# Kernel optimization log

Measured on AMD Instinct MI355X. Metric: run time of the kernel, lower is better.

## Reference

```python
import jax, jax.numpy as jnp
import numpy as np

INPUT_SIZE = 512
HIDDEN_SIZE = 1024
SEQ_LEN = 512
BATCH = 64

def _xavier(key, shape):
    fan_out, fan_in = shape
    bound = float(np.sqrt(6.0 / (fan_in + fan_out)))
    return jax.random.uniform(key, shape, jnp.float32, -bound, bound)

def setup_inputs() -> dict:
    key = jax.random.key(0)
    ks = jax.random.split(key, 5)
    return {
        "x_seq": jax.random.normal(ks[0], (SEQ_LEN, BATCH, INPUT_SIZE), jnp.float32),
        "h0": jax.random.normal(ks[1], (BATCH, HIDDEN_SIZE), jnp.float32),
        "U_c": _xavier(ks[2], (HIDDEN_SIZE, INPUT_SIZE)),
        "w_c": jnp.ones((HIDDEN_SIZE,), jnp.float32),
        "b_c": jnp.zeros((HIDDEN_SIZE,), jnp.float32),
        "U_a": _xavier(ks[3], (HIDDEN_SIZE, INPUT_SIZE)),
        "w_a": jnp.ones((HIDDEN_SIZE,), jnp.float32),
        "b_a": jnp.zeros((HIDDEN_SIZE,), jnp.float32),
        "U_h": _xavier(ks[4], (HIDDEN_SIZE, INPUT_SIZE)),
        "b_h": jnp.zeros((HIDDEN_SIZE,), jnp.float32),
    }

def reference(x_seq, h0, U_c, w_c, b_c, U_a, w_a, b_a, U_h, b_h):
    # Batch the three input projections across all timesteps (the compute-heavy
    # GEMMs), then run the inherently-sequential gated recurrence with lax.scan.
    xc = jnp.einsum('tbi,hi->tbh', x_seq, U_c) + b_c  # [T, B, H]
    xa = jnp.einsum('tbi,hi->tbh', x_seq, U_a) + b_a
    xh = jnp.einsum('tbi,hi->tbh', x_seq, U_h) + b_h

    def step(h, proj):
        pc, pa, ph = proj
        c = jax.nn.sigmoid(pc + w_c * h)
        a = 1.0 + jnp.tanh(pa + w_a * h)
        h_new = c * h + (1.0 - c) * jnp.tanh(ph + a * h)
        return h_new, h_new

    h_last, y_seq = jax.lax.scan(step, h0, (xc, xa, xh))
    return (y_seq, (h_last,))
```

## Files before the change

### kernel.cpp

```cpp
#include <hip/hip_runtime.h>
#include <cstdint>
#include <cstddef>

#define T_SEQ 512
#define BATCH 64
#define IN_SZ 512
#define HID   1024
#define BH    (BATCH*HID)
#define M_TOT (T_SEQ*BATCH)
#define D_CH  16

typedef float f32x4 __attribute__((ext_vector_type(4)));
typedef _Float16 f16x8 __attribute__((ext_vector_type(8)));

__device__ inline unsigned short f2h(float f){
  union { _Float16 h; unsigned short u; } v;
  v.h = (_Float16)f;
  return v.u;
}
__device__ inline float h2f(unsigned short s){
  union { unsigned short u; _Float16 h; } v; v.u = s;
  return (float)v.h;
}

__device__ inline float sigm_f(float x){ return 1.f/(1.f + __expf(-x)); }
__device__ inline float tanh_f(float x){ float e = __expf(2.f*x); return 1.f - 2.f/(e + 1.f); }

__device__ inline void async16(const void* g, void* l){
  __builtin_amdgcn_global_load_lds(
      (__attribute__((address_space(1))) void*)g,
      (__attribute__((address_space(3))) void*)l,
      16, 0, 0);
}

#define XBLK 16384
__global__ __launch_bounds__(256) void cvt_all(
    const float* __restrict__ x,  const float* __restrict__ Uc,
    const float* __restrict__ Ua, const float* __restrict__ Uh,
    unsigned short* __restrict__ xb, unsigned short* __restrict__ U0,
    unsigned short* __restrict__ U1, unsigned short* __restrict__ U2)
{
  int b = blockIdx.x;
  const float* in; unsigned short* out; int i;
  if (b < XBLK){
    in = x; out = xb; i = b*256 + threadIdx.x;
  } else {
    int r = b - XBLK;
    int which = r >> 9;
    int lb = r & 511;
    i = lb*256 + threadIdx.x;
    in  = (which==0) ? Uc : (which==1) ? Ua : Uh;
    out = (which==0) ? U0 : (which==1) ? U1 : U2;
  }
  float4 v = ((const float4*)in)[i];
  ushort4 o;
  o.x = f2h(v.x); o.y = f2h(v.y); o.z = f2h(v.z); o.w = f2h(v.w);
  ((ushort4*)out)[i] = o;
}

__global__ __launch_bounds__(256) void gemm3(
    const unsigned short* __restrict__ xb,
    const unsigned short* __restrict__ U0,
    const unsigned short* __restrict__ U1,
    const unsigned short* __restrict__ U2,
    const float* __restrict__ b0, const float* __restrict__ b1, const float* __restrict__ b2,
    unsigned short* out0, unsigned short* out1, void* out2, int ph_f16)
{
  __shared__ __align__(16) unsigned char smem_raw[34816];
  uint4* smem = (uint4*)smem_raw;
  unsigned short* strans = (unsigned short*)smem_raw;

  const int tid  = threadIdx.x;
  const int wave = tid >> 6, lane = tid & 63;
  const int quad = lane >> 4, l16 = lane & 15;

  const int bid  = blockIdx.x;
  const int xcd  = bid & 7;
  const int slot = bid >> 3;
  const int mbl  = slot / 24;
  const int inner = slot - mbl*24;
  const int mb = xcd*32 + mbl;
  const int z  = inner % 3;
  const int nb = inner / 3;

  const int m0 = mb * 128, n0 = nb * 128;
  const unsigned short* Um = (z==0) ? U0 : (z==1) ? U1 : U2;
  const float* bias        = (z==0) ? b0 : (z==1) ? b1 : b2;
  const int wm = wave >> 1, wn = wave & 1;

  const f32x4 zf = {0.f, 0.f, 0.f, 0.f};
  f32x4 acc[4][4];
#pragma unroll
  for (int i=0;i<4;i++)
#pragma unroll
    for (int j=0;j<4;j++) acc[i][j] = zf;

  const uint4* ldsA = smem;
  const uint4* ldsB = smem + 1024;

  for (int k0 = 0; k0 < IN_SZ; k0 += 64) {
#pragma unroll
    for (int j = 0; j < 4; j++) {
      int c   = (wave*4 + j)*64 + lane;
      int row = c >> 3;
      int og  = (c & 7) ^ (row & 7);
      const unsigned short* ga = xb + (size_t)(m0 + row)*IN_SZ + k0 + og*8;
      const unsigned short* gb = Um + (size_t)(n0 + row)*IN_SZ + k0 + og*8;
      async16(ga, (void*)(smem + (size_t)(wave*4 + j)*64));
      async16(gb, (void*)(smem + 1024 + (size_t)(wave*4 + j)*64));
    }
    __syncthreads();

#pragma unroll
    for (int ks8 = 0; ks8 < 8; ks8 += 4) {
      f16x8 af[4], bfr[4];
#pragma unroll
      for (int im = 0; im < 4; im++){
        int row = wm*64 + im*16 + l16;
        int ch  = row*8 + ((ks8 + quad) ^ (row & 7));
        af[im] = *(const f16x8*)(ldsA + ch);
      }
#pragma unroll
      for (int in = 0; in < 4; in++){
        int row = wn*64 + in*16 + l16;
        int ch  = row*8 + ((ks8 + quad) ^ (row & 7));
        bfr[in] = *(const f16x8*)(ldsB + ch);
      }
#pragma unroll
      for (int im = 0; im < 4; im++)
#pragma unroll
        for (int in = 0; in < 4; in++)
          acc[im][in] = __builtin_amdgcn_mfma_f32_16x16x32_f16(af[im], bfr[in], acc[im][in], 0, 0, 0);
    }
    __syncthreads();
  }

  float bv[4];
#pragma unroll
  for (int in = 0; in < 4; in++) bv[in] = bias[n0 + wn*64 + in*16 + l16];

  if (z == 2 && !ph_f16) {
    float* o32 = (float*)out2;
#pragma unroll
    for (int im = 0; im < 4; im++)
#pragma unroll
      for (int r = 0; r < 4; r++){
        int row = m0 + wm*64 + im*16 + quad*4 + r;
        size_t rb = (size_t)row * HID;
#pragma unroll
        for (int in = 0; in < 4; in++)
          o32[rb + n0 + wn*64 + in*16 + l16] = acc[im][in][r] + bv[in];
      }
    return;
  }

  unsigned short* op = (z==0) ? out0 : (z==1) ? out1 : (unsigned short*)out2;
  const int RS = 136;
#pragma unroll
  for (int im = 0; im < 4; im++)
#pragma unroll
    for (int r = 0; r < 4; r++){
      int row = wm*64 + im*16 + quad*4 + r;
#pragma unroll
      for (int in = 0; in < 4; in++){
        int col = wn*64 + in*16 + l16;
        strans[row*RS + col] = f2h(acc[im][in][r] + bv[in]);
      }
    }
  __syncthreads();
#pragma unroll
  for (int p = 0; p < 8; p++){
    int row = (tid >> 4) + p*16;
    int c8  = tid & 15;
    uint4 v = *(const uint4*)(strans + row*RS + c8*8);
    *(uint4*)(op + (size_t)(m0 + row)*HID + n0 + c8*8) = v;
  }
}

template <bool PH16>
__global__ __launch_bounds__(256) void scan_k(
    const unsigned short* __restrict__ pc, const unsigned short* __restrict__ pa,
    const void* __restrict__ phv,
    float* __restrict__ y,
    const float* __restrict__ h0, const float* __restrict__ wc, const float* __restrict__ wa,
    float* __restrict__ hlast)
{
  const int idx  = blockIdx.x * 256 + threadIdx.x;
  const int hidx = idx & (HID - 1);
  float h = h0[idx];
  const float wcv = wc[hidx], wav = wa[hidx];
  const unsigned short* ph16 = (const unsigned short*)phv;
  const float*          ph32 = (const float*)phv;

  unsigned short cpc[D_CH], cpa[D_CH];
  unsigned short npc[D_CH], npa[D_CH];
  float cph[D_CH], nph[D_CH];
  unsigned short cph16[D_CH], nph16[D_CH];

#pragma unroll
  for (int i = 0; i < D_CH; i++){
    size_t b = (size_t)i*BH + idx;
    cpc[i] = pc[b]; cpa[i] = pa[b];
    if (PH16) cph16[i] = ph16[b]; else cph[i] = ph32[b];
  }

  constexpr int NC = T_SEQ / D_CH;
  for (int c = 0; c < NC; c++){
    const int t0 = c * D_CH;
    if (c + 1 < NC){
#pragma unroll
      for (int i = 0; i < D_CH; i++){
        size_t b = (size_t)(t0 + D_CH + i)*BH + idx;
        npc[i] = pc[b]; npa[i] = pa[b];
        if (PH16) nph16[i] = ph16[b]; else nph[i] = ph32[b];
      }
    }
#pragma unroll
    for (int i = 0; i < D_CH; i++){
      float pcv = h2f(cpc[i]);
      float pav = h2f(cpa[i]);
      float phv_ = PH16 ? h2f(cph16[i]) : cph[i];
      float cc = sigm_f(pcv + wcv*h);
      float a  = 1.f + tanh_f(pav + wav*h);
      float hc = tanh_f(phv_ + a*h);
      h = cc*h + (1.f - cc)*hc;
      y[(size_t)(t0 + i)*BH + idx] = h;
    }
    if (c + 1 < NC){
#pragma unroll
      for (int i = 0; i < D_CH; i++){
        cpc[i] = npc[i]; cpa[i] = npa[i];
        if (PH16) cph16[i] = nph16[i]; else cph[i] = nph[i];
      }
    }
  }
  hlast[idx] = h;
}

extern "C" void kernel_launch(void* const* d_in, const int* in_sizes, int n_in,
                              void* d_out, int out_size, void* d_ws, size_t ws_size,
                              hipStream_t stream)
{
  const float* x  = (const float*)d_in[0];
  const float* h0 = (const float*)d_in[1];
  const float* Uc = (const float*)d_in[2];
  const float* wc = (const float*)d_in[3];
  const float* bc = (const float*)d_in[4];
  const float* Ua = (const float*)d_in[5];
  const float* wa = (const float*)d_in[6];
  const float* ba = (const float*)d_in[7];
  const float* Uh = (const float*)d_in[8];
  const float* bh = (const float*)d_in[9];

  float* y     = (float*)d_out;
  float* hlast = y + (size_t)T_SEQ * BH;

  const size_t szP16 = (size_t)T_SEQ * BH * 2;
  const size_t szX16 = (size_t)M_TOT * IN_SZ * 2;
  const size_t szU16 = (size_t)HID * IN_SZ * 2;

  const size_t base = 2*szP16 + szX16 + 3*szU16;
  const bool ph_sep = ws_size >= base + szP16;

  char* w = (char*)d_ws;
  unsigned short* pc16 = (unsigned short*)w;
  unsigned short* pa16 = (unsigned short*)(w + szP16);
  unsigned short* xb   = (unsigned short*)(w + 2*szP16);
  unsigned short* U0b  = (unsigned short*)(w + 2*szP16 + szX16);
  unsigned short* U1b  = U0b + szU16/2;
  unsigned short* U2b  = U1b + szU16/2;
  unsigned short* ph16 = (unsigned short*)(w + base);

  cvt_all<<<XBLK + 3*512, 256, 0, stream>>>(x, Uc, Ua, Uh, xb, U0b, U1b, U2b);

  void* phbuf = ph_sep ? (void*)ph16 : (void*)y;
  gemm3<<<6144, 256, 0, stream>>>(xb, U0b, U1b, U2b, bc, ba, bh,
                                  pc16, pa16, phbuf, ph_sep ? 1 : 0);

  if (ph_sep)
    scan_k<true><<<BH/256, 256, 0, stream>>>(pc16, pa16, (const void*)ph16,
                                             y, h0, wc, wa, hlast);
  else
    scan_k<false><<<BH/256, 256, 0, stream>>>(pc16, pa16, (const void*)y,
                                              y, h0, wc, wa, hlast);
}
```

Baseline: 436.3 us.

## Rewrite projection GEMM with 256x256 tiles and double-buffered async LDS pipeline

The three-way projection GEMM moves from 128x128 tiles with 4 waves and a load-then-compute loop to 256x256 tiles with 8 waves. The K loop is now split into half-tiles and double-buffered in 128KB of LDS, with explicit vmcnt waits, barriers and raised priority around MFMA clusters. This overlaps global loads with matrix math and raises data reuse per tile. The epilogue also changes to per-wave LDS staging without a block-wide sync. It relies on hand-tuned waitcnt counts, which are fragile, and the large LDS footprint limits occupancy.

```diff
diff --git a/kernel.cpp b/kernel.cpp
--- a/kernel.cpp
+++ b/kernel.cpp
@@ -58,7 +58,7 @@
   ((ushort4*)out)[i] = o;
 }
 
-__global__ __launch_bounds__(256) void gemm3(
+__global__ __launch_bounds__(512, 2) void gemm3(
     const unsigned short* __restrict__ xb,
     const unsigned short* __restrict__ U0,
     const unsigned short* __restrict__ U1,
@@ -66,9 +66,7 @@
     const float* __restrict__ b0, const float* __restrict__ b1, const float* __restrict__ b2,
     unsigned short* out0, unsigned short* out1, void* out2, int ph_f16)
 {
-  __shared__ __align__(16) unsigned char smem_raw[34816];
-  uint4* smem = (uint4*)smem_raw;
-  unsigned short* strans = (unsigned short*)smem_raw;
+  __shared__ __align__(16) unsigned char smem_raw[131072];
 
   const int tid  = threadIdx.x;
   const int wave = tid >> 6, lane = tid & 63;
@@ -77,103 +75,153 @@
   const int bid  = blockIdx.x;
   const int xcd  = bid & 7;
   const int slot = bid >> 3;
-  const int mbl  = slot / 24;
-  const int inner = slot - mbl*24;
-  const int mb = xcd*32 + mbl;
-  const int z  = inner % 3;
-  const int nb = inner / 3;
-
-  const int m0 = mb * 128, n0 = nb * 128;
+  const int mbl  = slot / 12;
+  const int inner= slot - mbl*12;
+  const int mb   = xcd*16 + mbl;
+  const int z    = inner % 3;
+  const int nb   = inner / 3;
+
+  const int m0 = mb * 256, n0 = nb * 256;
   const unsigned short* Um = (z==0) ? U0 : (z==1) ? U1 : U2;
   const float* bias        = (z==0) ? b0 : (z==1) ? b1 : b2;
-  const int wm = wave >> 1, wn = wave & 1;
+  const int wm = wave >> 2, wn = wave & 3;
+
+  const int laneRow = lane >> 2;
+  const int cg8     = ((lane & 3) ^ ((lane >> 3) & 3)) << 3;
+  const unsigned short* srcA = xb + (size_t)m0 * IN_SZ;
+  const unsigned short* srcB = Um + (size_t)n0 * IN_SZ;
+
+  const int cxa = l16*64 + ((quad ^ ((l16 >> 1) & 3)) << 4);
+
+  auto stageA = [&](int tile, int kh){
+    unsigned char* dst = smem_raw + (((tile & 1)*2 + kh) << 14);
+#pragma unroll
+    for (int j = 0; j < 2; ++j){
+      const unsigned short* g = srcA + (size_t)((wave*2 + j)*16 + laneRow)*IN_SZ
+                                + tile*64 + kh*32 + cg8;
+      async16(g, dst + (wave*2 + j)*1024);
+    }
+  };
+  auto stageB = [&](int tile, int kh){
+    unsigned char* dst = smem_raw + 65536 + (((tile & 1)*2 + kh) << 14);
+#pragma unroll
+    for (int j = 0; j < 2; ++j){
+      const unsigned short* g = srcB + (size_t)((wave*2 + j)*16 + laneRow)*IN_SZ
+                                + tile*64 + kh*32 + cg8;
+      async16(g, dst + (wave*2 + j)*1024);
+    }
+  };
 
   const f32x4 zf = {0.f, 0.f, 0.f, 0.f};
-  f32x4 acc[4][4];
-#pragma unroll
-  for (int i=0;i<4;i++)
-#pragma unroll
-    for (int j=0;j<4;j++) acc[i][j] = zf;
-
-  const uint4* ldsA = smem;
-  const uint4* ldsB = smem + 1024;
-
-  for (int k0 = 0; k0 < IN_SZ; k0 += 64) {
-#pragma unroll
-    for (int j = 0; j < 4; j++) {
-      int c   = (wave*4 + j)*64 + lane;
-      int row = c >> 3;
-      int og  = (c & 7) ^ (row & 7);
-      const unsigned short* ga = xb + (size_t)(m0 + row)*IN_SZ + k0 + og*8;
-      const unsigned short* gb = Um + (size_t)(n0 + row)*IN_SZ + k0 + og*8;
-      async16(ga, (void*)(smem + (size_t)(wave*4 + j)*64));
-      async16(gb, (void*)(smem + 1024 + (size_t)(wave*4 + j)*64));
-    }
-    __syncthreads();
-
-#pragma unroll
-    for (int ks8 = 0; ks8 < 8; ks8 += 4) {
-      f16x8 af[4], bfr[4];
-#pragma unroll
-      for (int im = 0; im < 4; im++){
-        int row = wm*64 + im*16 + l16;
-        int ch  = row*8 + ((ks8 + quad) ^ (row & 7));
-        af[im] = *(const f16x8*)(ldsA + ch);
-      }
-#pragma unroll
-      for (int in = 0; in < 4; in++){
-        int row = wn*64 + in*16 + l16;
-        int ch  = row*8 + ((ks8 + quad) ^ (row & 7));
-        bfr[in] = *(const f16x8*)(ldsB + ch);
-      }
-#pragma unroll
-      for (int im = 0; im < 4; im++)
-#pragma unroll
-        for (int in = 0; in < 4; in++)
-          acc[im][in] = __builtin_amdgcn_mfma_f32_16x16x32_f16(af[im], bfr[in], acc[im][in], 0, 0, 0);
-    }
-    __syncthreads();
-  }
+  f32x4 acc[8][4];
+#pragma unroll
+  for (int i = 0; i < 8; ++i)
+#pragma unroll
+    for (int j = 0; j < 4; ++j) acc[i][j] = zf;
+
+  stageA(0,0); stageB(0,0); stageA(0,1); stageB(0,1);
+  stageA(1,0); stageB(1,0); stageA(1,1);
+  asm volatile("s_waitcnt vmcnt(10)" ::: "memory");
+  __builtin_amdgcn_s_barrier();
+
+#define CLUSTER(B0_, B1_, N0_, N1_)                                                      \
+  __builtin_amdgcn_s_barrier();                                                          \
+  asm volatile("s_waitcnt lgkmcnt(0)" ::: "memory");                                     \
+  __builtin_amdgcn_s_setprio(1);                                                         \
+  _Pragma("unroll")                                                                      \
+  for (int im_ = 0; im_ < 8; ++im_){                                                     \
+    acc[im_][N0_] = __builtin_amdgcn_mfma_f32_16x16x32_f16(a0[im_], B0_, acc[im_][N0_], 0,0,0); \
+    acc[im_][N1_] = __builtin_amdgcn_mfma_f32_16x16x32_f16(a0[im_], B1_, acc[im_][N1_], 0,0,0); \
+  }                                                                                      \
+  __builtin_amdgcn_s_setprio(0);                                                         \
+  __builtin_amdgcn_s_barrier();
+
+  f16x8 a0[8];
+#pragma unroll
+  for (int g = 0; g < 8; ++g){
+    const int buf = g & 1;
+    const unsigned char* Ab0 = smem_raw + ((buf*2 + 0) << 14);
+    const unsigned char* Ab1 = smem_raw + ((buf*2 + 1) << 14);
+    const unsigned char* Bb0 = smem_raw + 65536 + ((buf*2 + 0) << 14);
+    const unsigned char* Bb1 = smem_raw + 65536 + ((buf*2 + 1) << 14);
+
+#pragma unroll
+    for (int im = 0; im < 8; ++im)
+      a0[im] = *(const f16x8*)(Ab0 + wm*8192 + im*1024 + cxa);
+    f16x8 q0 = *(const f16x8*)(Bb0 + wn*4096 + 0*1024 + cxa);
+    f16x8 q1 = *(const f16x8*)(Bb0 + wn*4096 + 1*1024 + cxa);
+    if (g < 7) stageB(g+1, 1);
+    CLUSTER(q0, q1, 0, 1)
+
+    f16x8 q2 = *(const f16x8*)(Bb0 + wn*4096 + 2*1024 + cxa);
+    f16x8 q3 = *(const f16x8*)(Bb0 + wn*4096 + 3*1024 + cxa);
+    if (g < 6) stageA(g+2, 0);
+    if (g < 6)      { asm volatile("s_waitcnt vmcnt(10)" ::: "memory"); }
+    else if (g == 6){ asm volatile("s_waitcnt vmcnt(8)"  ::: "memory"); }
+    else            { asm volatile("s_waitcnt vmcnt(0)"  ::: "memory"); }
+    CLUSTER(q2, q3, 2, 3)
+
+#pragma unroll
+    for (int im = 0; im < 8; ++im)
+      a0[im] = *(const f16x8*)(Ab1 + wm*8192 + im*1024 + cxa);
+    q0 = *(const f16x8*)(Bb1 + wn*4096 + 0*1024 + cxa);
+    q1 = *(const f16x8*)(Bb1 + wn*4096 + 1*1024 + cxa);
+    if (g < 6) stageB(g+2, 0);
+    CLUSTER(q0, q1, 0, 1)
+
+    q2 = *(const f16x8*)(Bb1 + wn*4096 + 2*1024 + cxa);
+    q3 = *(const f16x8*)(Bb1 + wn*4096 + 3*1024 + cxa);
+    if (g < 6) stageA(g+2, 1);
+    if (g < 6)      { asm volatile("s_waitcnt vmcnt(10)" ::: "memory"); }
+    else if (g == 6){ asm volatile("s_waitcnt vmcnt(4)"  ::: "memory"); }
+    CLUSTER(q2, q3, 2, 3)
+  }
+#undef CLUSTER
 
   float bv[4];
 #pragma unroll
-  for (int in = 0; in < 4; in++) bv[in] = bias[n0 + wn*64 + in*16 + l16];
+  for (int in = 0; in < 4; ++in) bv[in] = bias[n0 + wn*64 + in*16 + l16];
 
   if (z == 2 && !ph_f16) {
     float* o32 = (float*)out2;
 #pragma unroll
-    for (int im = 0; im < 4; im++)
-#pragma unroll
-      for (int r = 0; r < 4; r++){
-        int row = m0 + wm*64 + im*16 + quad*4 + r;
-        size_t rb = (size_t)row * HID;
-#pragma unroll
-        for (int in = 0; in < 4; in++)
+    for (int im = 0; im < 8; ++im)
+#pragma unroll
+      for (int r = 0; r < 4; ++r){
+        int grow = m0 + wm*128 + im*16 + quad*4 + r;
+        size_t rb = (size_t)grow * HID;
+#pragma unroll
+        for (int in = 0; in < 4; ++in)
           o32[rb + n0 + wn*64 + in*16 + l16] = acc[im][in][r] + bv[in];
       }
     return;
   }
 
   unsigned short* op = (z==0) ? out0 : (z==1) ? out1 : (unsigned short*)out2;
-  const int RS = 136;
-#pragma unroll
-  for (int im = 0; im < 4; im++)
-#pragma unroll
-    for (int r = 0; r < 4; r++){
-      int row = wm*64 + im*16 + quad*4 + r;
-#pragma unroll
-      for (int in = 0; in < 4; in++){
-        int col = wn*64 + in*16 + l16;
-        strans[row*RS + col] = f2h(acc[im][in][r] + bv[in]);
+  unsigned short* sw = (unsigned short*)smem_raw + wave*4608;
+#pragma unroll
+  for (int h = 0; h < 2; ++h){
+#pragma unroll
+    for (int i4 = 0; i4 < 4; ++i4){
+      int im = h*4 + i4;
+#pragma unroll
+      for (int r = 0; r < 4; ++r){
+        int lr = i4*16 + quad*4 + r;
+#pragma unroll
+        for (int in = 0; in < 4; ++in)
+          sw[lr*72 + in*16 + l16] = f2h(acc[im][in][r] + bv[in]);
       }
     }
-  __syncthreads();
-#pragma unroll
-  for (int p = 0; p < 8; p++){
-    int row = (tid >> 4) + p*16;
-    int c8  = tid & 15;
-    uint4 v = *(const uint4*)(strans + row*RS + c8*8);
-    *(uint4*)(op + (size_t)(m0 + row)*HID + n0 + c8*8) = v;
+    asm volatile("s_waitcnt lgkmcnt(0)" ::: "memory");
+#pragma unroll
+    for (int i = 0; i < 8; ++i){
+      int lr = i*8 + (lane >> 3);
+      int ch = lane & 7;
+      uint4 v = *(const uint4*)(sw + lr*72 + ch*8);
+      int grow = m0 + wm*128 + h*64 + lr;
+      *(uint4*)(op + (size_t)grow*HID + n0 + wn*64 + ch*8) = v;
+    }
+    if (h == 0) asm volatile("s_waitcnt lgkmcnt(0)" ::: "memory");
   }
 }
 
@@ -274,7 +322,7 @@
   cvt_all<<<XBLK + 3*512, 256, 0, stream>>>(x, Uc, Ua, Uh, xb, U0b, U1b, U2b);
 
   void* phbuf = ph_sep ? (void*)ph16 : (void*)y;
-  gemm3<<<6144, 256, 0, stream>>>(xb, U0b, U1b, U2b, bc, ba, bh,
+  gemm3<<<1536, 512, 0, stream>>>(xb, U0b, U1b, U2b, bc, ba, bh,
                                   pc16, pa16, phbuf, ph_sep ? 1 : 0);
 
   if (ph_sep)
```

After: 414.6 us. 1.05x faster.
